# Kernel tuning notes

Hardware: AMD Instinct MI355X
Metric: run time of the kernel (lower is better)

The kernel has to match this reference:

```python
import jax, jax.numpy as jnp
import numpy as np

V = 256      # vocab_size
DIM = 512    # d_model
K = 3        # kernel / patch size
E = max(8, DIM // (K * K))  # e_model = 56
B, L = 8, 8192
LN_EPS = 1e-5


def setup_inputs() -> dict:
    key = jax.random.key(0)
    ks = jax.random.split(key, 6)
    x = jax.random.randint(ks[0], (B, L, K, K), 0, V)
    emb_table = jax.random.normal(ks[1], (V, E), dtype=jnp.float32) * 0.02
    alpha = jax.random.uniform(ks[2], (1, 1, K, K), dtype=jnp.float32)
    conv_w = jax.random.normal(ks[3], (E, E, K, K), dtype=jnp.float32) * 0.05
    conv_b = jnp.zeros((E,), dtype=jnp.float32)
    proj_w = jax.random.normal(ks[4], (DIM, E * K * K), dtype=jnp.float32) * 0.02
    proj_b = jnp.zeros((DIM,), dtype=jnp.float32)
    gamma = jnp.ones((DIM,), dtype=jnp.float32)
    beta = jnp.zeros((DIM,), dtype=jnp.float32)
    return {"x": x, "emb_table": emb_table, "alpha": alpha,
            "conv_w": conv_w, "conv_b": conv_b,
            "proj_w": proj_w, "proj_b": proj_b,
            "gamma": gamma, "beta": beta}


def reference(x, emb_table, alpha, conv_w, conv_b, proj_w, proj_b, gamma, beta):
    b, l, m, n = x.shape
    # embedding lookup: [B*L, K, K, E]
    h = emb_table[x.reshape(b * l, m, n)]
    # to NCHW: [B*L, E, K, K]
    h = jnp.transpose(h, (0, 3, 1, 2))
    # 3x3 same-padding conv, E->E channels
    patch = jax.lax.conv_general_dilated(
        h, conv_w, window_strides=(1, 1), padding="SAME",
        dimension_numbers=("NCHW", "OIHW", "NCHW"))
    patch = patch + conv_b[None, :, None, None]
    # sigmoid-gated blend (alpha broadcasts over batch and channel)
    g = jax.nn.sigmoid(alpha)
    h = g * h + (1.0 - g) * patch
    # flatten channel-major (matches torch reshape on NCHW): [B*L, E*K*K]
    h = h.reshape(b * l, -1)
    # linear projection to d_model
    h = h @ proj_w.T + proj_b
    # layernorm over last dim
    mu = jnp.mean(h, axis=-1, keepdims=True)
    var = jnp.var(h, axis=-1, keepdims=True)
    h = (h - mu) * jax.lax.rsqrt(var + LN_EPS) * gamma + beta
    return h.reshape(b, l, -1)
```

## Files before the change

kernel.cpp:

```cpp
#include <hip/hip_runtime.h>

#define E_ 56
#define DIM_ 512
#define V_ 256
#define F_ 504
#define NROWS 65536

typedef float  vf4 __attribute__((ext_vector_type(4)));

__device__ __forceinline__ float sigmoidf_(float v) { return 1.0f / (1.0f + expf(-v)); }
__device__ __forceinline__ float bf_lo_(unsigned int u) {
  return __uint_as_float(u << 16);
}
__device__ __forceinline__ float bf_hi_(unsigned int u) {
  return __uint_as_float(u & 0xFFFF0000u);
}
__device__ __forceinline__ float bf2f_(unsigned short u) {
  return __uint_as_float(((unsigned int)u) << 16);
}
__device__ __forceinline__ unsigned short f2bf_(float f) {
  unsigned int b = __float_as_uint(f);
  b += 0x7FFFu + ((b >> 16) & 1u);
  return (unsigned short)(b >> 16);
}

__global__ __launch_bounds__(256) void k_trans(
    const float* __restrict__ proj_w,
    const float* __restrict__ conv_w,
    float* __restrict__ PW2,
    float* __restrict__ Ct)
{
  int idx = blockIdx.x * 256 + threadIdx.x;
  if (idx < 9 * DIM_ * E_) {
    int p = idx / (DIM_ * E_);
    int r = idx - p * (DIM_ * E_);
    int d = r / E_;
    int e = r - d * E_;
    PW2[idx] = proj_w[d * F_ + e * 9 + p];
  } else {
    int j = idx - 9 * DIM_ * E_;
    if (j >= E_ * 9 * E_) return;
    int c = j / (9 * E_);
    int r = j - c * (9 * E_);
    int k = r / E_;
    int e = r - k * E_;
    Ct[j] = conv_w[e * F_ + c * 9 + k];
  }
}

__global__ __launch_bounds__(256) void k_weff2(
    const float* __restrict__ proj_w,
    const float* __restrict__ PW2,
    const float* __restrict__ Ct,
    const float* __restrict__ alpha,
    float* __restrict__ Wt)
{
  int idx = blockIdx.x * 256 + threadIdx.x;
  int d = idx / F_;
  int f = idx - d * F_;
  int c = f / 9;
  int q = f - c * 9;
  int qi = q / 3, qj = q - qi * 3;
  float acc = sigmoidf_(alpha[q]) * proj_w[d * F_ + c * 9 + q];
  #pragma unroll
  for (int p = 0; p < 9; ++p) {
    int pi = p / 3, pj = p - pi * 3;
    int ki = qi - pi + 1, kj = qj - pj + 1;
    if (ki < 0 || ki > 2 || kj < 0 || kj > 2) continue;
    const vf4* A = (const vf4*)(PW2 + (p * DIM_ + d) * E_);
    const vf4* B = (const vf4*)(Ct + (c * 9 + (ki * 3 + kj)) * E_);
    vf4 sv = {0.f, 0.f, 0.f, 0.f};
    #pragma unroll
    for (int e4 = 0; e4 < E_ / 4; ++e4)
      sv += A[e4] * B[e4];
    float s = sv.x + sv.y + sv.z + sv.w;
    acc += (1.f - sigmoidf_(alpha[p])) * s;
  }
  Wt[(size_t)(q * E_ + c) * DIM_ + d] = acc;
}

__global__ __launch_bounds__(64) void k_beff_w(
    const float* __restrict__ proj_w,
    const float* __restrict__ conv_b,
    const float* __restrict__ proj_b,
    const float* __restrict__ alpha,
    float* __restrict__ beff)
{
  int d = blockIdx.x;
  int lane = threadIdx.x;
  const float* pr = proj_w + d * F_;
  float acc = 0.f;
  #pragma unroll
  for (int p = 0; p < 9; ++p) {
    float v = 0.f;
    if (lane < E_) v = pr[lane * 9 + p] * conv_b[lane];
    #pragma unroll
    for (int off = 32; off > 0; off >>= 1) v += __shfl_xor(v, off, 64);
    acc += (1.f - sigmoidf_(alpha[p])) * v;
  }
  if (lane == 0) beff[d] = proj_b[d] + acc;
}

__global__ __launch_bounds__(256) void k_tab8(
    const float* __restrict__ emb,
    const float* __restrict__ Wt,
    unsigned short* __restrict__ T)
{
  int q  = blockIdx.x >> 5;
  int t0 = (blockIdx.x & 31) * 8;
  int d0 = 2 * threadIdx.x;
  float a0[8], a1[8];
  #pragma unroll
  for (int j = 0; j < 8; ++j) { a0[j] = 0.f; a1[j] = 0.f; }
  for (int c = 0; c < E_; ++c) {
    float2 w = *(const float2*)(Wt + (size_t)(q * E_ + c) * DIM_ + d0);
    #pragma unroll
    for (int j = 0; j < 8; ++j) {
      float ev = emb[(t0 + j) * E_ + c];
      a0[j] += ev * w.x;
      a1[j] += ev * w.y;
    }
  }
  #pragma unroll
  for (int j = 0; j < 8; ++j) {
    size_t o = (size_t)((q << 8) + t0 + j) * DIM_ + d0;
    unsigned int u = (unsigned int)f2bf_(a0[j]) | ((unsigned int)f2bf_(a1[j]) << 16);
    *(unsigned int*)(T + o) = u;
  }
}

__device__ __forceinline__ void ln_reduce_(const float a[8], float& mu, float& rstd) {
  float s = 0.f, ss = 0.f;
  #pragma unroll
  for (int j = 0; j < 8; ++j) { s += a[j]; ss += a[j] * a[j]; }
  #pragma unroll
  for (int off = 32; off > 0; off >>= 1) {
    s  += __shfl_xor(s, off, 64);
    ss += __shfl_xor(ss, off, 64);
  }
  mu = s * (1.0f / 512.0f);
  float var = ss * (1.0f / 512.0f) - mu * mu;
  rstd = rsqrtf(var + 1e-5f);
}

__global__ __launch_bounds__(256) void k_main_bf(
    const int*            __restrict__ x,
    const unsigned short* __restrict__ T,
    const float* __restrict__ beff,
    const float* __restrict__ gamma,
    const float* __restrict__ beta,
    float* __restrict__ out)
{
  int row = __builtin_amdgcn_readfirstlane((blockIdx.x * 256 + threadIdx.x) >> 6);
  int lane = threadIdx.x & 63;
  const int* __restrict__ xr = x + row * 9;

  uint4 u[9];
  #pragma unroll
  for (int q = 0; q < 9; ++q) {
    int t = xr[q];
    u[q] = *((const uint4*)(T + (size_t)((q << 8) + t) * DIM_) + lane);
  }

  const float4* b4 = (const float4*)beff;
  float4 B0 = b4[2 * lane], B1 = b4[2 * lane + 1];
  float a[8] = {B0.x, B0.y, B0.z, B0.w, B1.x, B1.y, B1.z, B1.w};

  #pragma unroll
  for (int q = 0; q < 9; ++q) {
    a[0] += bf_lo_(u[q].x); a[1] += bf_hi_(u[q].x);
    a[2] += bf_lo_(u[q].y); a[3] += bf_hi_(u[q].y);
    a[4] += bf_lo_(u[q].z); a[5] += bf_hi_(u[q].z);
    a[6] += bf_lo_(u[q].w); a[7] += bf_hi_(u[q].w);
  }

  float mu, rstd;
  ln_reduce_(a, mu, rstd);

  const float4* g4  = (const float4*)gamma;
  const float4* be4 = (const float4*)beta;
  float4 G0 = g4[2 * lane], G1 = g4[2 * lane + 1];
  float4 P0 = be4[2 * lane], P1 = be4[2 * lane + 1];

  vf4 o0, o1;
  o0.x = (a[0] - mu) * rstd * G0.x + P0.x;
  o0.y = (a[1] - mu) * rstd * G0.y + P0.y;
  o0.z = (a[2] - mu) * rstd * G0.z + P0.z;
  o0.w = (a[3] - mu) * rstd * G0.w + P0.w;
  o1.x = (a[4] - mu) * rstd * G1.x + P1.x;
  o1.y = (a[5] - mu) * rstd * G1.y + P1.y;
  o1.z = (a[6] - mu) * rstd * G1.z + P1.z;
  o1.w = (a[7] - mu) * rstd * G1.w + P1.w;

  vf4* o4 = (vf4*)(out + (size_t)row * DIM_ + lane * 8);
  __builtin_nontemporal_store(o0, o4);
  __builtin_nontemporal_store(o1, o4 + 1);
}

__global__ __launch_bounds__(256) void k_weff_bf(
    const float* __restrict__ proj_w,
    const float* __restrict__ conv_w,
    const float* __restrict__ alpha,
    unsigned short* __restrict__ Wt)
{
  int idx = blockIdx.x * 256 + threadIdx.x;
  int d = idx / F_;
  int f = idx - d * F_;
  int c = f / 9;
  int q = f - c * 9;
  int qi = q / 3, qj = q - qi * 3;
  const float* pr = proj_w + d * F_;
  float acc = sigmoidf_(alpha[q]) * pr[c * 9 + q];
  for (int pi = 0; pi < 3; ++pi) {
    for (int pj = 0; pj < 3; ++pj) {
      int ki = qi - pi + 1, kj = qj - pj + 1;
      if (ki < 0 || ki > 2 || kj < 0 || kj > 2) continue;
      int p = pi * 3 + pj;
      const float* cwp = conv_w + c * 9 + (ki * 3 + kj);
      const float* prp = pr + p;
      float s = 0.f;
      #pragma unroll 8
      for (int e = 0; e < E_; ++e)
        s += prp[e * 9] * cwp[e * F_];
      acc += (1.f - sigmoidf_(alpha[p])) * s;
    }
  }
  Wt[(size_t)(q * E_ + c) * DIM_ + d] = f2bf_(acc);
}

__global__ __launch_bounds__(256) void k_init(
    const float* __restrict__ beff, float* __restrict__ out)
{
  int idx = blockIdx.x * 256 + threadIdx.x;
  ((float4*)out)[idx] = ((const float4*)beff)[idx & 127];
}

__global__ __launch_bounds__(256) void k_accq(
    const int* __restrict__ x,
    const float* __restrict__ emb,
    const unsigned short* __restrict__ Wt,
    float* __restrict__ out, int q)
{
  const int tid = threadIdx.x;
  const int d = blockIdx.y * 256 + tid;
  const int row0 = blockIdx.x * 512;
  const unsigned short* wq = Wt + (size_t)(q * E_) * DIM_ + d;

  for (int rb = 0; rb < 512; rb += 8) {
    int tv[8]; float a[8];
    #pragma unroll
    for (int j = 0; j < 8; ++j) {
      tv[j] = x[(size_t)(row0 + rb + j) * 9 + q];
      a[j] = 0.f;
    }
    for (int c = 0; c < E_; ++c) {
      float w = bf2f_(wq[(size_t)c * DIM_]);
      #pragma unroll
      for (int j = 0; j < 8; ++j)
        a[j] += emb[tv[j] * E_ + c] * w;
    }
    #pragma unroll
    for (int j = 0; j < 8; ++j) {
      size_t o = (size_t)(row0 + rb + j) * DIM_ + d;
      out[o] += a[j];
    }
  }
}

__global__ __launch_bounds__(256) void k_ln(
    const float* __restrict__ gamma, const float* __restrict__ beta,
    float* __restrict__ out)
{
  int gid = blockIdx.x * 256 + threadIdx.x;
  int row = gid >> 6;
  int lane = threadIdx.x & 63;
  float* op = out + (size_t)row * DIM_ + lane * 8;
  float4 A0 = *(float4*)op, A1 = *(float4*)(op + 4);
  float a[8] = {A0.x, A0.y, A0.z, A0.w, A1.x, A1.y, A1.z, A1.w};
  float mu, rstd;
  ln_reduce_(a, mu, rstd);
  const float4* g4  = (const float4*)gamma;
  const float4* be4 = (const float4*)beta;
  float4 G0 = g4[2 * lane], G1 = g4[2 * lane + 1];
  float4 P0 = be4[2 * lane], P1 = be4[2 * lane + 1];
  float4 o0, o1;
  o0.x = (a[0] - mu) * rstd * G0.x + P0.x;
  o0.y = (a[1] - mu) * rstd * G0.y + P0.y;
  o0.z = (a[2] - mu) * rstd * G0.z + P0.z;
  o0.w = (a[3] - mu) * rstd * G0.w + P0.w;
  o1.x = (a[4] - mu) * rstd * G1.x + P1.x;
  o1.y = (a[5] - mu) * rstd * G1.y + P1.y;
  o1.z = (a[6] - mu) * rstd * G1.z + P1.z;
  o1.w = (a[7] - mu) * rstd * G1.w + P1.w;
  *(float4*)op = o0;
  *(float4*)(op + 4) = o1;
}

extern "C" void kernel_launch(void* const* d_in, const int* in_sizes, int n_in,
                              void* d_out, int out_size, void* d_ws, size_t ws_size,
                              hipStream_t stream) {
  const int*   x      = (const int*)  d_in[0];
  const float* emb    = (const float*)d_in[1];
  const float* alpha  = (const float*)d_in[2];
  const float* conv_w = (const float*)d_in[3];
  const float* conv_b = (const float*)d_in[4];
  const float* proj_w = (const float*)d_in[5];
  const float* proj_b = (const float*)d_in[6];
  const float* gamma  = (const float*)d_in[7];
  const float* beta   = (const float*)d_in[8];
  float* out = (float*)d_out;

  float* beff = (float*)d_ws;
  char* wsbase = (char*)d_ws;

  const size_t OFF_WT  = 2048;
  const size_t OFF_T   = OFF_WT + (size_t)9 * E_ * DIM_ * 4;
  const size_t OFF_PW2 = OFF_T  + (size_t)9 * V_ * DIM_ * 2;
  const size_t OFF_CT  = OFF_PW2 + (size_t)9 * DIM_ * E_ * 4;
  const size_t needMain = OFF_CT + (size_t)E_ * 9 * E_ * 4;

  hipLaunchKernelGGL(k_beff_w, dim3(DIM_), dim3(64), 0, stream,
                     proj_w, conv_b, proj_b, alpha, beff);

  if (ws_size >= needMain) {
    float* Wt  = (float*)(wsbase + OFF_WT);
    unsigned short* T = (unsigned short*)(wsbase + OFF_T);
    float* PW2 = (float*)(wsbase + OFF_PW2);
    float* Ct  = (float*)(wsbase + OFF_CT);
    hipLaunchKernelGGL(k_trans, dim3(1119), dim3(256), 0, stream,
                       proj_w, conv_w, PW2, Ct);
    hipLaunchKernelGGL(k_weff2, dim3((DIM_ * F_) / 256), dim3(256), 0, stream,
                       proj_w, PW2, Ct, alpha, Wt);
    hipLaunchKernelGGL(k_tab8, dim3(9 * 32), dim3(256), 0, stream,
                       emb, Wt, T);
    hipLaunchKernelGGL(k_main_bf, dim3(NROWS / 4), dim3(256), 0, stream,
                       x, T, beff, gamma, beta, out);
  } else {
    unsigned short* Wt = (unsigned short*)(wsbase + 2048);
    hipLaunchKernelGGL(k_weff_bf, dim3((DIM_ * F_) / 256), dim3(256), 0, stream,
                       proj_w, conv_w, alpha, Wt);
    hipLaunchKernelGGL(k_init, dim3((NROWS * DIM_ / 4) / 256), dim3(256), 0, stream,
                       beff, out);
    for (int q = 0; q < 9; ++q)
      hipLaunchKernelGGL(k_accq, dim3(128, 2), dim3(256), 0, stream,
                         x, emb, Wt, out, q);
    hipLaunchKernelGGL(k_ln, dim3(NROWS / 4), dim3(256), 0, stream,
                       gamma, beta, out);
  }
}
```

Measured before the change: 105.0 us.

## Restructure weight-folding precompute and prefetch table rows across four rows per wave

The effective-weight precompute now transposes proj_w once to a d-contiguous layout. A new kernel computes each output as a coalesced float2-per-thread accumulation over conv weights, replacing the earlier per-element dot-product kernel and its extra transposes. The main gather+LayerNorm kernel now has each wave handle four rows and prefetch the nine bf16 table rows for the next row while reducing the current one, so gather latency can overlap with the reduction. This raises register pressure and cuts the number of blocks by four, which may lower occupancy. The weight-folding kernel also launches only 126 blocks.

```diff
diff --git a/kernel.cpp b/kernel.cpp
--- a/kernel.cpp
+++ b/kernel.cpp
@@ -24,59 +24,60 @@
   return (unsigned short)(b >> 16);
 }
 
-__global__ __launch_bounds__(256) void k_trans(
+__global__ __launch_bounds__(256) void k_trans_pt(
     const float* __restrict__ proj_w,
+    float* __restrict__ PT)
+{
+  int idx = blockIdx.x * 256 + threadIdx.x;
+  int f = idx >> 9;
+  int d = idx & 511;
+  PT[idx] = proj_w[d * F_ + f];
+}
+
+__global__ __launch_bounds__(256) void k_weff3(
+    const float* __restrict__ PT,
     const float* __restrict__ conv_w,
-    float* __restrict__ PW2,
-    float* __restrict__ Ct)
-{
-  int idx = blockIdx.x * 256 + threadIdx.x;
-  if (idx < 9 * DIM_ * E_) {
-    int p = idx / (DIM_ * E_);
-    int r = idx - p * (DIM_ * E_);
-    int d = r / E_;
-    int e = r - d * E_;
-    PW2[idx] = proj_w[d * F_ + e * 9 + p];
-  } else {
-    int j = idx - 9 * DIM_ * E_;
-    if (j >= E_ * 9 * E_) return;
-    int c = j / (9 * E_);
-    int r = j - c * (9 * E_);
-    int k = r / E_;
-    int e = r - k * E_;
-    Ct[j] = conv_w[e * F_ + c * 9 + k];
-  }
-}
-
-__global__ __launch_bounds__(256) void k_weff2(
-    const float* __restrict__ proj_w,
-    const float* __restrict__ PW2,
-    const float* __restrict__ Ct,
     const float* __restrict__ alpha,
     float* __restrict__ Wt)
 {
-  int idx = blockIdx.x * 256 + threadIdx.x;
-  int d = idx / F_;
-  int f = idx - d * F_;
-  int c = f / 9;
-  int q = f - c * 9;
+  int b = blockIdx.x;
+  int q = b / 14;
+  int c0 = (b - q * 14) * 4;
   int qi = q / 3, qj = q - qi * 3;
-  float acc = sigmoidf_(alpha[q]) * proj_w[d * F_ + c * 9 + q];
+  int d0 = threadIdx.x * 2;
+
+  float g[9];
+  #pragma unroll
+  for (int p = 0; p < 9; ++p) g[p] = sigmoidf_(alpha[p]);
+
+  float2 acc[4];
+  #pragma unroll
+  for (int j = 0; j < 4; ++j) {
+    float2 v = *(const float2*)(PT + (((c0 + j) * 9 + q) << 9) + d0);
+    acc[j].x = g[q] * v.x;
+    acc[j].y = g[q] * v.y;
+  }
+
   #pragma unroll
   for (int p = 0; p < 9; ++p) {
     int pi = p / 3, pj = p - pi * 3;
     int ki = qi - pi + 1, kj = qj - pj + 1;
     if (ki < 0 || ki > 2 || kj < 0 || kj > 2) continue;
-    const vf4* A = (const vf4*)(PW2 + (p * DIM_ + d) * E_);
-    const vf4* B = (const vf4*)(Ct + (c * 9 + (ki * 3 + kj)) * E_);
-    vf4 sv = {0.f, 0.f, 0.f, 0.f};
-    #pragma unroll
-    for (int e4 = 0; e4 < E_ / 4; ++e4)
-      sv += A[e4] * B[e4];
-    float s = sv.x + sv.y + sv.z + sv.w;
-    acc += (1.f - sigmoidf_(alpha[p])) * s;
-  }
-  Wt[(size_t)(q * E_ + c) * DIM_ + d] = acc;
+    int kk = ki * 3 + kj;
+    float wp = 1.f - g[p];
+    for (int e = 0; e < E_; ++e) {
+      float2 row = *(const float2*)(PT + (((e * 9 + p)) << 9) + d0);
+      #pragma unroll
+      for (int j = 0; j < 4; ++j) {
+        float cw = wp * conv_w[e * F_ + (c0 + j) * 9 + kk];
+        acc[j].x += cw * row.x;
+        acc[j].y += cw * row.y;
+      }
+    }
+  }
+  #pragma unroll
+  for (int j = 0; j < 4; ++j)
+    *(float2*)(Wt + ((size_t)(q * E_ + c0 + j) << 9) + d0) = acc[j];
 }
 
 __global__ __launch_bounds__(64) void k_beff_w(
@@ -143,7 +144,7 @@
   rstd = rsqrtf(var + 1e-5f);
 }
 
-__global__ __launch_bounds__(256) void k_main_bf(
+__global__ __launch_bounds__(256) void k_main4(
     const int*            __restrict__ x,
     const unsigned short* __restrict__ T,
     const float* __restrict__ beff,
@@ -151,50 +152,62 @@
     const float* __restrict__ beta,
     float* __restrict__ out)
 {
-  int row = __builtin_amdgcn_readfirstlane((blockIdx.x * 256 + threadIdx.x) >> 6);
   int lane = threadIdx.x & 63;
-  const int* __restrict__ xr = x + row * 9;
-
-  uint4 u[9];
-  #pragma unroll
-  for (int q = 0; q < 9; ++q) {
-    int t = xr[q];
-    u[q] = *((const uint4*)(T + (size_t)((q << 8) + t) * DIM_) + lane);
-  }
-
-  const float4* b4 = (const float4*)beff;
-  float4 B0 = b4[2 * lane], B1 = b4[2 * lane + 1];
-  float a[8] = {B0.x, B0.y, B0.z, B0.w, B1.x, B1.y, B1.z, B1.w};
-
-  #pragma unroll
-  for (int q = 0; q < 9; ++q) {
-    a[0] += bf_lo_(u[q].x); a[1] += bf_hi_(u[q].x);
-    a[2] += bf_lo_(u[q].y); a[3] += bf_hi_(u[q].y);
-    a[4] += bf_lo_(u[q].z); a[5] += bf_hi_(u[q].z);
-    a[6] += bf_lo_(u[q].w); a[7] += bf_hi_(u[q].w);
-  }
-
-  float mu, rstd;
-  ln_reduce_(a, mu, rstd);
-
+  int wid  = __builtin_amdgcn_readfirstlane(threadIdx.x >> 6);
+  int row0 = blockIdx.x * 16 + wid * 4;
+  const int* __restrict__ xr = x + row0 * 9;
+
+  const float4* b4  = (const float4*)beff;
   const float4* g4  = (const float4*)gamma;
   const float4* be4 = (const float4*)beta;
-  float4 G0 = g4[2 * lane], G1 = g4[2 * lane + 1];
+  float4 C0 = b4[2 * lane],  C1 = b4[2 * lane + 1];
+  float4 G0 = g4[2 * lane],  G1 = g4[2 * lane + 1];
   float4 P0 = be4[2 * lane], P1 = be4[2 * lane + 1];
 
-  vf4 o0, o1;
-  o0.x = (a[0] - mu) * rstd * G0.x + P0.x;
-  o0.y = (a[1] - mu) * rstd * G0.y + P0.y;
-  o0.z = (a[2] - mu) * rstd * G0.z + P0.z;
-  o0.w = (a[3] - mu) * rstd * G0.w + P0.w;
-  o1.x = (a[4] - mu) * rstd * G1.x + P1.x;
-  o1.y = (a[5] - mu) * rstd * G1.y + P1.y;
-  o1.z = (a[6] - mu) * rstd * G1.z + P1.z;
-  o1.w = (a[7] - mu) * rstd * G1.w + P1.w;
-
-  vf4* o4 = (vf4*)(out + (size_t)row * DIM_ + lane * 8);
-  __builtin_nontemporal_store(o0, o4);
-  __builtin_nontemporal_store(o1, o4 + 1);
+  uint4 cur[9], nxt[9];
+  #pragma unroll
+  for (int q = 0; q < 9; ++q)
+    cur[q] = *((const uint4*)(T + (size_t)((q << 8) + xr[q]) * DIM_) + lane);
+
+  #pragma unroll
+  for (int r = 0; r < 4; ++r) {
+    if (r < 3) {
+      #pragma unroll
+      for (int q = 0; q < 9; ++q)
+        nxt[q] = *((const uint4*)(T + (size_t)((q << 8) + xr[(r + 1) * 9 + q]) * DIM_) + lane);
+    }
+
+    float a[8] = {C0.x, C0.y, C0.z, C0.w, C1.x, C1.y, C1.z, C1.w};
+    #pragma unroll
+    for (int q = 0; q < 9; ++q) {
+      a[0] += bf_lo_(cur[q].x); a[1] += bf_hi_(cur[q].x);
+      a[2] += bf_lo_(cur[q].y); a[3] += bf_hi_(cur[q].y);
+      a[4] += bf_lo_(cur[q].z); a[5] += bf_hi_(cur[q].z);
+      a[6] += bf_lo_(cur[q].w); a[7] += bf_hi_(cur[q].w);
+    }
+
+    float mu, rstd;
+    ln_reduce_(a, mu, rstd);
+
+    vf4 o0, o1;
+    o0.x = (a[0] - mu) * rstd * G0.x + P0.x;
+    o0.y = (a[1] - mu) * rstd * G0.y + P0.y;
+    o0.z = (a[2] - mu) * rstd * G0.z + P0.z;
+    o0.w = (a[3] - mu) * rstd * G0.w + P0.w;
+    o1.x = (a[4] - mu) * rstd * G1.x + P1.x;
+    o1.y = (a[5] - mu) * rstd * G1.y + P1.y;
+    o1.z = (a[6] - mu) * rstd * G1.z + P1.z;
+    o1.w = (a[7] - mu) * rstd * G1.w + P1.w;
+
+    vf4* o4 = (vf4*)(out + (size_t)(row0 + r) * DIM_ + lane * 8);
+    __builtin_nontemporal_store(o0, o4);
+    __builtin_nontemporal_store(o1, o4 + 1);
+
+    if (r < 3) {
+      #pragma unroll
+      for (int q = 0; q < 9; ++q) cur[q] = nxt[q];
+    }
+  }
 }
 
 __global__ __launch_bounds__(256) void k_weff_bf(
@@ -315,9 +328,8 @@
 
   const size_t OFF_WT  = 2048;
   const size_t OFF_T   = OFF_WT + (size_t)9 * E_ * DIM_ * 4;
-  const size_t OFF_PW2 = OFF_T  + (size_t)9 * V_ * DIM_ * 2;
-  const size_t OFF_CT  = OFF_PW2 + (size_t)9 * DIM_ * E_ * 4;
-  const size_t needMain = OFF_CT + (size_t)E_ * 9 * E_ * 4;
+  const size_t OFF_PT  = OFF_T  + (size_t)9 * V_ * DIM_ * 2;
+  const size_t needMain = OFF_PT + (size_t)F_ * DIM_ * 4;
 
   hipLaunchKernelGGL(k_beff_w, dim3(DIM_), dim3(64), 0, stream,
                      proj_w, conv_b, proj_b, alpha, beff);
@@ -325,15 +337,14 @@
   if (ws_size >= needMain) {
     float* Wt  = (float*)(wsbase + OFF_WT);
     unsigned short* T = (unsigned short*)(wsbase + OFF_T);
-    float* PW2 = (float*)(wsbase + OFF_PW2);
-    float* Ct  = (float*)(wsbase + OFF_CT);
-    hipLaunchKernelGGL(k_trans, dim3(1119), dim3(256), 0, stream,
-                       proj_w, conv_w, PW2, Ct);
-    hipLaunchKernelGGL(k_weff2, dim3((DIM_ * F_) / 256), dim3(256), 0, stream,
-                       proj_w, PW2, Ct, alpha, Wt);
+    float* PT  = (float*)(wsbase + OFF_PT);
+    hipLaunchKernelGGL(k_trans_pt, dim3(1008), dim3(256), 0, stream,
+                       proj_w, PT);
+    hipLaunchKernelGGL(k_weff3, dim3(126), dim3(256), 0, stream,
+                       PT, conv_w, alpha, Wt);
     hipLaunchKernelGGL(k_tab8, dim3(9 * 32), dim3(256), 0, stream,
                        emb, Wt, T);
-    hipLaunchKernelGGL(k_main_bf, dim3(NROWS / 4), dim3(256), 0, stream,
+    hipLaunchKernelGGL(k_main4, dim3(NROWS / 16), dim3(256), 0, stream,
                        x, T, beff, gamma, beta, out);
   } else {
     unsigned short* Wt = (unsigned short*)(wsbase + 2048);
```

After: 122.6 us. +16.8%, slower.

## Split main pass into LDS-sliced table gather plus separate bf16 layernorm pass

Applied to the files above, without the earlier changes.

Replaces the fused gather+layernorm kernel with three stages. Tokens are packed to bytes, and the per-position lookup table is re-laid out into 8-column slices that each block holds in LDS. Each block gathers and sums the 9 table entries for its slice into a bf16 intermediate buffer. A separate kernel then does layernorm and writes the output with nontemporal stores. The aim is to turn scattered global table reads into LDS reads. The cost is an extra 64 MB bf16 round trip through global memory plus two more launches, which needs a larger workspace.

```diff
diff --git a/kernel.cpp b/kernel.cpp
--- a/kernel.cpp
+++ b/kernel.cpp
@@ -99,6 +99,150 @@
     acc += (1.f - sigmoidf_(alpha[p])) * v;
   }
   if (lane == 0) beff[d] = proj_b[d] + acc;
+}
+
+__global__ __launch_bounds__(256) void k_tab8s(
+    const float* __restrict__ emb,
+    const float* __restrict__ Wt,
+    unsigned int* __restrict__ Tsl)
+{
+  int q  = blockIdx.x >> 5;
+  int t0 = (blockIdx.x & 31) * 8;
+  int tid = threadIdx.x;
+  int d0 = 2 * tid;
+  float a0[8], a1[8];
+  #pragma unroll
+  for (int j = 0; j < 8; ++j) { a0[j] = 0.f; a1[j] = 0.f; }
+  for (int c = 0; c < E_; ++c) {
+    float2 w = *(const float2*)(Wt + (size_t)(q * E_ + c) * DIM_ + d0);
+    #pragma unroll
+    for (int j = 0; j < 8; ++j) {
+      float ev = emb[(t0 + j) * E_ + c];
+      a0[j] += ev * w.x;
+      a1[j] += ev * w.y;
+    }
+  }
+  int s = tid >> 2, dl2 = tid & 3;
+  #pragma unroll
+  for (int j = 0; j < 8; ++j) {
+    unsigned int u = (unsigned int)f2bf_(a0[j]) | ((unsigned int)f2bf_(a1[j]) << 16);
+    Tsl[((size_t)(s * 9 + q) * 256 + (t0 + j)) * 4 + dl2] = u;
+  }
+}
+
+__global__ __launch_bounds__(256) void k_packx(
+    const int* __restrict__ x, unsigned int* __restrict__ x8)
+{
+  int row = blockIdx.x * 256 + threadIdx.x;
+  const int* xr = x + row * 9;
+  unsigned int w0 = (xr[0] & 255) | ((xr[1] & 255) << 8) |
+                    ((xr[2] & 255) << 16) | ((unsigned int)(xr[3] & 255) << 24);
+  unsigned int w1 = (xr[4] & 255) | ((xr[5] & 255) << 8) |
+                    ((xr[6] & 255) << 16) | ((unsigned int)(xr[7] & 255) << 24);
+  unsigned int w2 = (xr[8] & 255);
+  x8[row * 3 + 0] = w0;
+  x8[row * 3 + 1] = w1;
+  x8[row * 3 + 2] = w2;
+}
+
+__global__ __launch_bounds__(256) void k_gather(
+    const unsigned int* __restrict__ x8,
+    const unsigned int* __restrict__ Tsl,
+    const float* __restrict__ beff,
+    unsigned int* __restrict__ h2)
+{
+  __shared__ __align__(16) unsigned int tl[9216];
+  int s   = blockIdx.x;
+  int rb  = blockIdx.y;
+  int tid = threadIdx.x;
+
+  const uint4* src = (const uint4*)(Tsl + (size_t)s * 9216);
+  uint4* dst = (uint4*)tl;
+  #pragma unroll
+  for (int k = 0; k < 9; ++k)
+    dst[tid + k * 256] = src[tid + k * 256];
+  __syncthreads();
+
+  int dl2  = tid & 3;
+  int rloc = tid >> 2;
+  float2 bv = *(const float2*)(beff + s * 8 + dl2 * 2);
+  int row0 = rb * 2048;
+
+  for (int it = 0; it < 32; ++it) {
+    int row = row0 + it * 64 + rloc;
+    const unsigned int* xr = x8 + row * 3;
+    unsigned int w0 = xr[0], w1 = xr[1], w2 = xr[2];
+    float a0 = bv.x, a1 = bv.y;
+    #pragma unroll
+    for (int q = 0; q < 9; ++q) {
+      unsigned int wq = (q < 4) ? w0 : ((q < 8) ? w1 : w2);
+      unsigned int tok = (wq >> ((q & 3) * 8)) & 255u;
+      unsigned int v = tl[(q * 256 + tok) * 4 + dl2];
+      a0 += bf_lo_(v);
+      a1 += bf_hi_(v);
+    }
+    unsigned int hv = (unsigned int)f2bf_(a0) | ((unsigned int)f2bf_(a1) << 16);
+    h2[(size_t)(row >> 2) * 1024 + s * 16 + (row & 3) * 4 + dl2] = hv;
+  }
+}
+
+__global__ __launch_bounds__(256) void k_lnb(
+    const unsigned int* __restrict__ h2,
+    const float* __restrict__ gamma,
+    const float* __restrict__ beta,
+    float* __restrict__ out)
+{
+  int i = threadIdx.x & 63;
+  int w = threadIdx.x >> 6;
+  int g = blockIdx.x * 4 + w;
+
+  const uint4* hp = (const uint4*)(h2 + (size_t)g * 1024);
+  uint4 hv[4];
+  #pragma unroll
+  for (int k = 0; k < 4; ++k) hv[k] = hp[k * 64 + i];
+
+  float af[32];
+  #pragma unroll
+  for (int k = 0; k < 4; ++k) {
+    af[k * 8 + 0] = bf_lo_(hv[k].x); af[k * 8 + 1] = bf_hi_(hv[k].x);
+    af[k * 8 + 2] = bf_lo_(hv[k].y); af[k * 8 + 3] = bf_hi_(hv[k].y);
+    af[k * 8 + 4] = bf_lo_(hv[k].z); af[k * 8 + 5] = bf_hi_(hv[k].z);
+    af[k * 8 + 6] = bf_lo_(hv[k].w); af[k * 8 + 7] = bf_hi_(hv[k].w);
+  }
+
+  float s1 = 0.f, ss = 0.f;
+  #pragma unroll
+  for (int j = 0; j < 32; ++j) { s1 += af[j]; ss += af[j] * af[j]; }
+  #pragma unroll
+  for (int off = 4; off <= 32; off <<= 1) {
+    s1 += __shfl_xor(s1, off, 64);
+    ss += __shfl_xor(ss, off, 64);
+  }
+  float mu   = s1 * (1.0f / 512.0f);
+  float var  = ss * (1.0f / 512.0f) - mu * mu;
+  float rstd = rsqrtf(var + 1e-5f);
+
+  int row = g * 4 + (i & 3);
+  const float4* g4  = (const float4*)gamma;
+  const float4* be4 = (const float4*)beta;
+  #pragma unroll
+  for (int k = 0; k < 4; ++k) {
+    int s = k * 16 + (i >> 2);
+    float4 G0 = g4[s * 2],  G1 = g4[s * 2 + 1];
+    float4 B0 = be4[s * 2], B1 = be4[s * 2 + 1];
+    vf4 o0, o1;
+    o0.x = (af[k*8+0] - mu) * rstd * G0.x + B0.x;
+    o0.y = (af[k*8+1] - mu) * rstd * G0.y + B0.y;
+    o0.z = (af[k*8+2] - mu) * rstd * G0.z + B0.z;
+    o0.w = (af[k*8+3] - mu) * rstd * G0.w + B0.w;
+    o1.x = (af[k*8+4] - mu) * rstd * G1.x + B1.x;
+    o1.y = (af[k*8+5] - mu) * rstd * G1.y + B1.y;
+    o1.z = (af[k*8+6] - mu) * rstd * G1.z + B1.z;
+    o1.w = (af[k*8+7] - mu) * rstd * G1.w + B1.w;
+    vf4* o4 = (vf4*)(out + (size_t)row * DIM_ + s * 8);
+    __builtin_nontemporal_store(o0, o4);
+    __builtin_nontemporal_store(o1, o4 + 1);
+  }
 }
 
 __global__ __launch_bounds__(256) void k_tab8(
@@ -314,19 +458,40 @@
   char* wsbase = (char*)d_ws;
 
   const size_t OFF_WT  = 2048;
-  const size_t OFF_T   = OFF_WT + (size_t)9 * E_ * DIM_ * 4;
-  const size_t OFF_PW2 = OFF_T  + (size_t)9 * V_ * DIM_ * 2;
+  const size_t OFF_PW2 = OFF_WT  + (size_t)9 * E_ * DIM_ * 4;
   const size_t OFF_CT  = OFF_PW2 + (size_t)9 * DIM_ * E_ * 4;
-  const size_t needMain = OFF_CT + (size_t)E_ * 9 * E_ * 4;
+  const size_t OFF_X8  = OFF_CT  + (size_t)E_ * 9 * E_ * 4;
+  const size_t OFF_TSL = OFF_X8  + (size_t)NROWS * 12;
+  const size_t OFF_H2  = OFF_TSL + (size_t)9 * V_ * DIM_ * 2;
+  const size_t need2   = OFF_H2  + (size_t)NROWS * DIM_ * 2;
+  const size_t need1   = OFF_H2;
 
   hipLaunchKernelGGL(k_beff_w, dim3(DIM_), dim3(64), 0, stream,
                      proj_w, conv_b, proj_b, alpha, beff);
 
-  if (ws_size >= needMain) {
+  if (ws_size >= need2) {
     float* Wt  = (float*)(wsbase + OFF_WT);
-    unsigned short* T = (unsigned short*)(wsbase + OFF_T);
     float* PW2 = (float*)(wsbase + OFF_PW2);
     float* Ct  = (float*)(wsbase + OFF_CT);
+    unsigned int* x8  = (unsigned int*)(wsbase + OFF_X8);
+    unsigned int* Tsl = (unsigned int*)(wsbase + OFF_TSL);
+    unsigned int* h2  = (unsigned int*)(wsbase + OFF_H2);
+    hipLaunchKernelGGL(k_trans, dim3(1119), dim3(256), 0, stream,
+                       proj_w, conv_w, PW2, Ct);
+    hipLaunchKernelGGL(k_packx, dim3(NROWS / 256), dim3(256), 0, stream, x, x8);
+    hipLaunchKernelGGL(k_weff2, dim3((DIM_ * F_) / 256), dim3(256), 0, stream,
+                       proj_w, PW2, Ct, alpha, Wt);
+    hipLaunchKernelGGL(k_tab8s, dim3(9 * 32), dim3(256), 0, stream,
+                       emb, Wt, Tsl);
+    hipLaunchKernelGGL(k_gather, dim3(64, 32), dim3(256), 0, stream,
+                       x8, Tsl, beff, h2);
+    hipLaunchKernelGGL(k_lnb, dim3(NROWS / 16), dim3(256), 0, stream,
+                       h2, gamma, beta, out);
+  } else if (ws_size >= need1) {
+    float* Wt  = (float*)(wsbase + OFF_WT);
+    float* PW2 = (float*)(wsbase + OFF_PW2);
+    float* Ct  = (float*)(wsbase + OFF_CT);
+    unsigned short* T = (unsigned short*)(wsbase + OFF_TSL);
     hipLaunchKernelGGL(k_trans, dim3(1119), dim3(256), 0, stream,
                        proj_w, conv_w, PW2, Ct);
     hipLaunchKernelGGL(k_weff2, dim3((DIM_ * F_) / 256), dim3(256), 0, stream,
```

After: 170.6 us. 1.62x slower.

## Merge bias prep into transpose kernel, fold bias into table, pipeline 4 rows per wave

Applied to the files above, without the earlier changes.

The bias-computation kernel is merged into the transpose pre-pass, saving one launch. The effective bias, divided by 9, is folded into each of the nine lookup-table slices, so the main kernel no longer loads or adds it. The main kernel now has each wave process 4 rows with software prefetch of the next row's nine table gathers, and loads gamma and beta once per wave. Folding the bias into the bf16 table adds a small rounding error, and the larger grid per wave adds register pressure.

```diff
diff --git a/kernel.cpp b/kernel.cpp
--- a/kernel.cpp
+++ b/kernel.cpp
@@ -24,27 +24,47 @@
   return (unsigned short)(b >> 16);
 }
 
-__global__ __launch_bounds__(256) void k_trans(
+__global__ __launch_bounds__(256) void k_pre(
     const float* __restrict__ proj_w,
     const float* __restrict__ conv_w,
+    const float* __restrict__ conv_b,
+    const float* __restrict__ proj_b,
+    const float* __restrict__ alpha,
     float* __restrict__ PW2,
-    float* __restrict__ Ct)
-{
-  int idx = blockIdx.x * 256 + threadIdx.x;
-  if (idx < 9 * DIM_ * E_) {
+    float* __restrict__ Ct,
+    float* __restrict__ beff)
+{
+  int b = blockIdx.x;
+  if (b < 1008) {
+    int idx = b * 256 + threadIdx.x;
     int p = idx / (DIM_ * E_);
     int r = idx - p * (DIM_ * E_);
     int d = r / E_;
     int e = r - d * E_;
     PW2[idx] = proj_w[d * F_ + e * 9 + p];
+  } else if (b < 1119) {
+    int j = (b - 1008) * 256 + threadIdx.x;
+    if (j < E_ * 9 * E_) {
+      int c = j / (9 * E_);
+      int r = j - c * (9 * E_);
+      int k = r / E_;
+      int e = r - k * E_;
+      Ct[j] = conv_w[e * F_ + c * 9 + k];
+    }
   } else {
-    int j = idx - 9 * DIM_ * E_;
-    if (j >= E_ * 9 * E_) return;
-    int c = j / (9 * E_);
-    int r = j - c * (9 * E_);
-    int k = r / E_;
-    int e = r - k * E_;
-    Ct[j] = conv_w[e * F_ + c * 9 + k];
+    int d = (b - 1119) * 4 + (threadIdx.x >> 6);
+    int lane = threadIdx.x & 63;
+    const float* pr = proj_w + d * F_;
+    float acc = 0.f;
+    #pragma unroll
+    for (int p = 0; p < 9; ++p) {
+      float v = 0.f;
+      if (lane < E_) v = pr[lane * 9 + p] * conv_b[lane];
+      #pragma unroll
+      for (int off = 32; off > 0; off >>= 1) v += __shfl_xor(v, off, 64);
+      acc += (1.f - sigmoidf_(alpha[p])) * v;
+    }
+    if (lane == 0) beff[d] = proj_b[d] + acc;
   }
 }
 
@@ -79,39 +99,21 @@
   Wt[(size_t)(q * E_ + c) * DIM_ + d] = acc;
 }
 
-__global__ __launch_bounds__(64) void k_beff_w(
-    const float* __restrict__ proj_w,
-    const float* __restrict__ conv_b,
-    const float* __restrict__ proj_b,
-    const float* __restrict__ alpha,
-    float* __restrict__ beff)
-{
-  int d = blockIdx.x;
-  int lane = threadIdx.x;
-  const float* pr = proj_w + d * F_;
-  float acc = 0.f;
-  #pragma unroll
-  for (int p = 0; p < 9; ++p) {
-    float v = 0.f;
-    if (lane < E_) v = pr[lane * 9 + p] * conv_b[lane];
-    #pragma unroll
-    for (int off = 32; off > 0; off >>= 1) v += __shfl_xor(v, off, 64);
-    acc += (1.f - sigmoidf_(alpha[p])) * v;
-  }
-  if (lane == 0) beff[d] = proj_b[d] + acc;
-}
-
-__global__ __launch_bounds__(256) void k_tab8(
+__global__ __launch_bounds__(256) void k_tab8b(
     const float* __restrict__ emb,
     const float* __restrict__ Wt,
+    const float* __restrict__ beff,
     unsigned short* __restrict__ T)
 {
   int q  = blockIdx.x >> 5;
   int t0 = (blockIdx.x & 31) * 8;
   int d0 = 2 * threadIdx.x;
+  const float inv9 = 1.0f / 9.0f;
+  float2 bv = *(const float2*)(beff + d0);
+  float b0 = bv.x * inv9, b1 = bv.y * inv9;
   float a0[8], a1[8];
   #pragma unroll
-  for (int j = 0; j < 8; ++j) { a0[j] = 0.f; a1[j] = 0.f; }
+  for (int j = 0; j < 8; ++j) { a0[j] = b0; a1[j] = b1; }
   for (int c = 0; c < E_; ++c) {
     float2 w = *(const float2*)(Wt + (size_t)(q * E_ + c) * DIM_ + d0);
     #pragma unroll
@@ -143,58 +145,67 @@
   rstd = rsqrtf(var + 1e-5f);
 }
 
-__global__ __launch_bounds__(256) void k_main_bf(
+__global__ __launch_bounds__(256) void k_main4b(
     const int*            __restrict__ x,
     const unsigned short* __restrict__ T,
-    const float* __restrict__ beff,
     const float* __restrict__ gamma,
     const float* __restrict__ beta,
     float* __restrict__ out)
 {
-  int row = __builtin_amdgcn_readfirstlane((blockIdx.x * 256 + threadIdx.x) >> 6);
   int lane = threadIdx.x & 63;
-  const int* __restrict__ xr = x + row * 9;
-
-  uint4 u[9];
-  #pragma unroll
-  for (int q = 0; q < 9; ++q) {
-    int t = xr[q];
-    u[q] = *((const uint4*)(T + (size_t)((q << 8) + t) * DIM_) + lane);
-  }
-
-  const float4* b4 = (const float4*)beff;
-  float4 B0 = b4[2 * lane], B1 = b4[2 * lane + 1];
-  float a[8] = {B0.x, B0.y, B0.z, B0.w, B1.x, B1.y, B1.z, B1.w};
-
-  #pragma unroll
-  for (int q = 0; q < 9; ++q) {
-    a[0] += bf_lo_(u[q].x); a[1] += bf_hi_(u[q].x);
-    a[2] += bf_lo_(u[q].y); a[3] += bf_hi_(u[q].y);
-    a[4] += bf_lo_(u[q].z); a[5] += bf_hi_(u[q].z);
-    a[6] += bf_lo_(u[q].w); a[7] += bf_hi_(u[q].w);
-  }
-
-  float mu, rstd;
-  ln_reduce_(a, mu, rstd);
+  int wid  = __builtin_amdgcn_readfirstlane(threadIdx.x >> 6);
+  int row0 = blockIdx.x * 16 + wid * 4;
+  const int* __restrict__ xr = x + row0 * 9;
 
   const float4* g4  = (const float4*)gamma;
   const float4* be4 = (const float4*)beta;
-  float4 G0 = g4[2 * lane], G1 = g4[2 * lane + 1];
+  float4 G0 = g4[2 * lane],  G1 = g4[2 * lane + 1];
   float4 P0 = be4[2 * lane], P1 = be4[2 * lane + 1];
 
-  vf4 o0, o1;
-  o0.x = (a[0] - mu) * rstd * G0.x + P0.x;
-  o0.y = (a[1] - mu) * rstd * G0.y + P0.y;
-  o0.z = (a[2] - mu) * rstd * G0.z + P0.z;
-  o0.w = (a[3] - mu) * rstd * G0.w + P0.w;
-  o1.x = (a[4] - mu) * rstd * G1.x + P1.x;
-  o1.y = (a[5] - mu) * rstd * G1.y + P1.y;
-  o1.z = (a[6] - mu) * rstd * G1.z + P1.z;
-  o1.w = (a[7] - mu) * rstd * G1.w + P1.w;
-
-  vf4* o4 = (vf4*)(out + (size_t)row * DIM_ + lane * 8);
-  __builtin_nontemporal_store(o0, o4);
-  __builtin_nontemporal_store(o1, o4 + 1);
+  uint4 cur[9], nxt[9];
+  #pragma unroll
+  for (int q = 0; q < 9; ++q)
+    cur[q] = *((const uint4*)(T + (size_t)((q << 8) + xr[q]) * DIM_) + lane);
+
+  #pragma unroll
+  for (int r = 0; r < 4; ++r) {
+    if (r < 3) {
+      #pragma unroll
+      for (int q = 0; q < 9; ++q)
+        nxt[q] = *((const uint4*)(T + (size_t)((q << 8) + xr[(r + 1) * 9 + q]) * DIM_) + lane);
+    }
+
+    float a[8] = {0.f, 0.f, 0.f, 0.f, 0.f, 0.f, 0.f, 0.f};
+    #pragma unroll
+    for (int q = 0; q < 9; ++q) {
+      a[0] += bf_lo_(cur[q].x); a[1] += bf_hi_(cur[q].x);
+      a[2] += bf_lo_(cur[q].y); a[3] += bf_hi_(cur[q].y);
+      a[4] += bf_lo_(cur[q].z); a[5] += bf_hi_(cur[q].z);
+      a[6] += bf_lo_(cur[q].w); a[7] += bf_hi_(cur[q].w);
+    }
+
+    float mu, rstd;
+    ln_reduce_(a, mu, rstd);
+
+    vf4 o0, o1;
+    o0.x = (a[0] - mu) * rstd * G0.x + P0.x;
+    o0.y = (a[1] - mu) * rstd * G0.y + P0.y;
+    o0.z = (a[2] - mu) * rstd * G0.z + P0.z;
+    o0.w = (a[3] - mu) * rstd * G0.w + P0.w;
+    o1.x = (a[4] - mu) * rstd * G1.x + P1.x;
+    o1.y = (a[5] - mu) * rstd * G1.y + P1.y;
+    o1.z = (a[6] - mu) * rstd * G1.z + P1.z;
+    o1.w = (a[7] - mu) * rstd * G1.w + P1.w;
+
+    vf4* o4 = (vf4*)(out + (size_t)(row0 + r) * DIM_ + lane * 8);
+    __builtin_nontemporal_store(o0, o4);
+    __builtin_nontemporal_store(o1, o4 + 1);
+
+    if (r < 3) {
+      #pragma unroll
+      for (int q = 0; q < 9; ++q) cur[q] = nxt[q];
+    }
+  }
 }
 
 __global__ __launch_bounds__(256) void k_weff_bf(
@@ -226,6 +237,28 @@
     }
   }
   Wt[(size_t)(q * E_ + c) * DIM_ + d] = f2bf_(acc);
+}
+
+__global__ __launch_bounds__(64) void k_beff_w(
+    const float* __restrict__ proj_w,
+    const float* __restrict__ conv_b,
+    const float* __restrict__ proj_b,
+    const float* __restrict__ alpha,
+    float* __restrict__ beff)
+{
+  int d = blockIdx.x;
+  int lane = threadIdx.x;
+  const float* pr = proj_w + d * F_;
+  float acc = 0.f;
+  #pragma unroll
+  for (int p = 0; p < 9; ++p) {
+    float v = 0.f;
+    if (lane < E_) v = pr[lane * 9 + p] * conv_b[lane];
+    #pragma unroll
+    for (int off = 32; off > 0; off >>= 1) v += __shfl_xor(v, off, 64);
+    acc += (1.f - sigmoidf_(alpha[p])) * v;
+  }
+  if (lane == 0) beff[d] = proj_b[d] + acc;
 }
 
 __global__ __launch_bounds__(256) void k_init(
@@ -314,29 +347,28 @@
   char* wsbase = (char*)d_ws;
 
   const size_t OFF_WT  = 2048;
-  const size_t OFF_T   = OFF_WT + (size_t)9 * E_ * DIM_ * 4;
-  const size_t OFF_PW2 = OFF_T  + (size_t)9 * V_ * DIM_ * 2;
+  const size_t OFF_PW2 = OFF_WT  + (size_t)9 * E_ * DIM_ * 4;
   const size_t OFF_CT  = OFF_PW2 + (size_t)9 * DIM_ * E_ * 4;
-  const size_t needMain = OFF_CT + (size_t)E_ * 9 * E_ * 4;
-
-  hipLaunchKernelGGL(k_beff_w, dim3(DIM_), dim3(64), 0, stream,
-                     proj_w, conv_b, proj_b, alpha, beff);
+  const size_t OFF_T   = OFF_CT  + (size_t)E_ * 9 * E_ * 4;
+  const size_t needMain = OFF_T + (size_t)9 * V_ * DIM_ * 2;
 
   if (ws_size >= needMain) {
     float* Wt  = (float*)(wsbase + OFF_WT);
-    unsigned short* T = (unsigned short*)(wsbase + OFF_T);
     float* PW2 = (float*)(wsbase + OFF_PW2);
     float* Ct  = (float*)(wsbase + OFF_CT);
-    hipLaunchKernelGGL(k_trans, dim3(1119), dim3(256), 0, stream,
-                       proj_w, conv_w, PW2, Ct);
+    unsigned short* T = (unsigned short*)(wsbase + OFF_T);
+    hipLaunchKernelGGL(k_pre, dim3(1247), dim3(256), 0, stream,
+                       proj_w, conv_w, conv_b, proj_b, alpha, PW2, Ct, beff);
     hipLaunchKernelGGL(k_weff2, dim3((DIM_ * F_) / 256), dim3(256), 0, stream,
                        proj_w, PW2, Ct, alpha, Wt);
-    hipLaunchKernelGGL(k_tab8, dim3(9 * 32), dim3(256), 0, stream,
-                       emb, Wt, T);
-    hipLaunchKernelGGL(k_main_bf, dim3(NROWS / 4), dim3(256), 0, stream,
-                       x, T, beff, gamma, beta, out);
+    hipLaunchKernelGGL(k_tab8b, dim3(9 * 32), dim3(256), 0, stream,
+                       emb, Wt, beff, T);
+    hipLaunchKernelGGL(k_main4b, dim3(NROWS / 16), dim3(256), 0, stream,
+                       x, T, gamma, beta, out);
   } else {
     unsigned short* Wt = (unsigned short*)(wsbase + 2048);
+    hipLaunchKernelGGL(k_beff_w, dim3(DIM_), dim3(64), 0, stream,
+                       proj_w, conv_b, proj_b, alpha, beff);
     hipLaunchKernelGGL(k_weff_bf, dim3((DIM_ * F_) / 256), dim3(256), 0, stream,
                        proj_w, conv_w, alpha, Wt);
     hipLaunchKernelGGL(k_init, dim3((NROWS * DIM_ / 4) / 256), dim3(256), 0, stream,
```

New measurement: 100.9 us (median of 2 runs). 3.9% less time.
